# Kernel tuning notes

Measured on AMD Instinct MI355X. Metric: run time of the kernel, lower is better.

The kernel has to match this reference:

```python
import jax, jax.numpy as jnp
import numpy as np

GAMMA = 0.5

def _rbf_gram(a, b):
    # exp(-gamma * ||a - b||^2), computed via the expanded quadratic form.
    # a: [N, d], b: [M, d] -> [N, M]
    a2 = jnp.sum(a * a, axis=-1)                      # [N]
    b2 = jnp.sum(b * b, axis=-1)                      # [M]
    sq = a2[:, None] + b2[None, :] - 2.0 * (a @ b.T)  # [N, M]
    return jnp.exp(-GAMMA * jnp.maximum(sq, 0.0))


def setup_inputs() -> dict:
    key = jax.random.key(0)
    kx, kp = jax.random.split(key)
    x = jax.random.normal(kx, (32768, 16), dtype=jnp.float32)
    particles = jax.random.normal(kp, (8192, 16), dtype=jnp.float32)
    return {"x": x, "particles": particles}


def reference(x, particles):
    n_p = particles.shape[0]
    # p=None, norm=True -> px = ones(N_x) / N_x
    px = jnp.ones(x.shape[0], dtype=x.dtype) / x.shape[0]
    t1 = jnp.mean(_rbf_gram(particles, particles))           # mean over [N_p, N_p]
    t2 = 2.0 * jnp.sum(px @ _rbf_gram(x, particles)) / n_p   # weighted row-sum of [N_x, N_p]
    return t1 - t2
```

## Files before the change

### kernel.cpp

```cpp
#include <hip/hip_runtime.h>
#include <hip/hip_bf16.h>

#define THREADS 256
#define DIM 16

typedef __attribute__((ext_vector_type(8))) short bf16x8;
typedef __attribute__((ext_vector_type(16))) float f32x16;
typedef __attribute__((ext_vector_type(2))) float f32x2;

__device__ __forceinline__ float rawexp2(float a) { return __builtin_amdgcn_exp2f(a); }

__global__ __launch_bounds__(THREADS) void prep_kernel(
    const float* __restrict__ x, int nx,
    const float* __restrict__ p, int np,
    short* __restrict__ xbs, float* __restrict__ xn,
    short* __restrict__ pbs, short* __restrict__ pb,
    float* __restrict__ pn, float* __restrict__ pfp)
{
    const float L2E  = 1.44269504088896340736f;
    const float HL2E = 0.72134752044448170368f;
    int i = blockIdx.x * THREADS + threadIdx.x;
    const float* src; short* ds; short* dp; float* dn; float* df;
    if (i < nx) {
        src = x + (size_t)i * DIM; ds = xbs + (size_t)i * DIM;
        dp = nullptr; dn = xn + i; df = nullptr;
    } else if (i < nx + np) {
        int j = i - nx;
        src = p + (size_t)j * DIM; ds = pbs + (size_t)j * DIM;
        dp = pb + (size_t)j * DIM; dn = pn + j; df = pfp + j;
    } else {
        return;
    }

    float nrm = 0.f;
    bf16x8 plo, phi, slo, shi;
#pragma unroll
    for (int k = 0; k < DIM; ++k) {
        unsigned u = __float_as_uint(src[k]);
        unsigned short r = (unsigned short)((u + 0x7FFFu + ((u >> 16) & 1u)) >> 16);
        float fr = __uint_as_float((unsigned)r << 16);
        nrm = fmaf(fr, fr, nrm);
        unsigned us = __float_as_uint(L2E * fr);
        unsigned short rs = (unsigned short)((us + 0x7FFFu + ((us >> 16) & 1u)) >> 16);
        if (k < 8) { plo[k] = (short)r; slo[k] = (short)rs; }
        else       { phi[k - 8] = (short)r; shi[k - 8] = (short)rs; }
    }
    *(bf16x8*)ds = slo; *((bf16x8*)ds + 1) = shi;
    if (dp) { *(bf16x8*)dp = plo; *((bf16x8*)dp + 1) = phi; }
    float ns = -HL2E * nrm;
    *dn = ns;
    if (df) *df = rawexp2(ns);
}

__device__ __forceinline__ void consume_tile(const f32x16& d, float f, f32x2& acc)
{
    f32x2 e0 = { rawexp2(d[0]),  rawexp2(d[1])  };
    f32x2 e1 = { rawexp2(d[2]),  rawexp2(d[3])  };
    f32x2 e2 = { rawexp2(d[4]),  rawexp2(d[5])  };
    f32x2 e3 = { rawexp2(d[6]),  rawexp2(d[7])  };
    f32x2 e4 = { rawexp2(d[8]),  rawexp2(d[9])  };
    f32x2 e5 = { rawexp2(d[10]), rawexp2(d[11]) };
    f32x2 e6 = { rawexp2(d[12]), rawexp2(d[13]) };
    f32x2 e7 = { rawexp2(d[14]), rawexp2(d[15]) };

    f32x2 s0 = e0 + e1;
    f32x2 s1 = e2 + e3;
    f32x2 s2 = e4 + e5;
    f32x2 s3 = e6 + e7;
    f32x2 u0 = s0 + s1;
    f32x2 u1 = s2 + s3;
    f32x2 t  = u0 + u1;
    f32x2 pf2 = {f, f};
    acc = t * pf2 + acc;
}

__device__ __forceinline__ float gram_phase(
    const short* __restrict__ rowsb, const float* __restrict__ rown,
    const short* __restrict__ colsb, const float* __restrict__ colpf,
    int row0, int ct0, int ntiles, int l31, int half)
{
    bf16x8 afrag = *(const bf16x8*)(rowsb + (size_t)(row0 + l31) * DIM + half * 8);

    f32x16 cseed;
#pragma unroll
    for (int r = 0; r < 16; ++r) {
        int rrow = (r & 3) + 8 * (r >> 2) + 4 * half;
        cseed[r] = rown[row0 + rrow];
    }

    const short* bptr = colsb + ((size_t)ct0 * 32 + l31) * DIM + half * 8;
    const float* fptr = colpf + ct0 * 32 + l31;
    const size_t bstride = (size_t)32 * DIM;

    bf16x8 b0 = *(const bf16x8*)bptr;
    bf16x8 b1 = *(const bf16x8*)(bptr + bstride);
    float  f0 = fptr[0];
    float  f1 = fptr[32];

    f32x16 d0 = __builtin_amdgcn_mfma_f32_32x32x16_bf16(afrag, b0, cseed, 0, 0, 0);
    f32x16 d1 = __builtin_amdgcn_mfma_f32_32x32x16_bf16(afrag, b1, cseed, 0, 0, 0);

    f32x2 acc = {0.f, 0.f};

#pragma unroll 1
    for (int t = 0; t + 2 < ntiles; t += 2) {
        bf16x8 bn0 = *(const bf16x8*)(bptr + (size_t)(t + 2) * bstride);
        float  fn0 = fptr[(t + 2) * 32];
        bf16x8 bn1 = *(const bf16x8*)(bptr + (size_t)(t + 3) * bstride);
        float  fn1 = fptr[(t + 3) * 32];

        consume_tile(d0, f0, acc);
        d0 = __builtin_amdgcn_mfma_f32_32x32x16_bf16(afrag, bn0, cseed, 0, 0, 0);
        consume_tile(d1, f1, acc);
        d1 = __builtin_amdgcn_mfma_f32_32x32x16_bf16(afrag, bn1, cseed, 0, 0, 0);

        f0 = fn0; f1 = fn1;
    }
    consume_tile(d0, f0, acc);
    consume_tile(d1, f1, acc);
    return acc.x + acc.y;
}

__device__ __forceinline__ void tri_run(
    const short* __restrict__ rowsb, const float* __restrict__ rown,
    const short* __restrict__ colsb, const float* __restrict__ colpf,
    int rt, int ct0, int len, bool diagFirst, int l31, int half,
    f32x2& accD, f32x2& accU)
{
    if (len <= 0) return;
    const int row0 = rt * 32;
    bf16x8 afrag = *(const bf16x8*)(rowsb + (size_t)(row0 + l31) * DIM + half * 8);

    f32x16 cseed;
#pragma unroll
    for (int r = 0; r < 16; ++r) {
        int rrow = (r & 3) + 8 * (r >> 2) + 4 * half;
        cseed[r] = rown[row0 + rrow];
    }

    const short* bptr = colsb + ((size_t)ct0 * 32 + l31) * DIM + half * 8;
    const float* fptr = colpf + ct0 * 32 + l31;
    const size_t bstride = (size_t)32 * DIM;

    bf16x8 bC = *(const bf16x8*)bptr;
    float  fC = fptr[0];
    f32x16 d = __builtin_amdgcn_mfma_f32_32x32x16_bf16(afrag, bC, cseed, 0, 0, 0);

#pragma unroll 1
    for (int t = 0; t < len; ++t) {
        bf16x8 bN; float fN;
        if (t + 1 < len) {
            bN = *(const bf16x8*)(bptr + (size_t)(t + 1) * bstride);
            fN = fptr[(t + 1) * 32];
        }
        if (diagFirst && t == 0) {
            consume_tile(d, fC, accD);
        } else {
            consume_tile(d, fC, accU);
        }
        if (t + 1 < len) {
            d = __builtin_amdgcn_mfma_f32_32x32x16_bf16(afrag, bN, cseed, 0, 0, 0);
            fC = fN;
        }
    }
}

__global__ __launch_bounds__(THREADS) void gram_fused_kernel(
    const short* __restrict__ xbs, const float* __restrict__ xn,
    const short* __restrict__ pbs, const short* __restrict__ pb,
    const float* __restrict__ pn, const float* __restrict__ pfp,
    double sc1, double sc2,
    double* __restrict__ partials)
{
    const int lane = threadIdx.x & 63;
    const int wv   = threadIdx.x >> 6;
    const int l31  = lane & 31;
    const int half = lane >> 5;
    const int w    = blockIdx.x * (THREADS / 64) + wv;

    f32x2 accD = {0.f, 0.f}, accU = {0.f, 0.f};
    {
        const int j = w >> 5;
        const int k = w & 31;
        const int s   = (k == 0) ? 0 : 8 * k + 1;
        const int cnt = (k == 0) ? 9 : 8;
        const int m = 256 - j;

        {
            const int lo = s;
            const int hi = (s + cnt < m) ? (s + cnt) : m;
            const int lenA = hi - lo;
            if (lenA > 0)
                tri_run(pbs, pn, pb, pfp, j, j + lo, lenA, lo == 0,
                        l31, half, accD, accU);
        }
        {
            const int lo = (s > m) ? s : m;
            const int hi = s + cnt;
            const int lenB = hi - lo;
            if (lenB > 0) {
                const int i2 = lo - m;
                tri_run(pbs, pn, pb, pfp, 255 - j, (255 - j) + i2, lenB,
                        i2 == 0, l31, half, accD, accU);
            }
        }
    }
    float t1d = accD.x + accD.y;
    float t1u = accU.x + accU.y;

    const int rt2 = w & 1023;
    const int c20 = (w >> 10) * 64;
    float acc2 = gram_phase(xbs, xn, pb, pfp, rt2 * 32, c20, 64, l31, half);

    double v = ((double)t1d + 2.0 * (double)t1u) * sc1
             - (double)acc2 * sc2;
#pragma unroll
    for (int off = 32; off > 0; off >>= 1) v += __shfl_down(v, off);

    __shared__ double sred[THREADS / 64];
    if (lane == 0) sred[wv] = v;
    __syncthreads();
    if (threadIdx.x == 0) {
        double tot = 0.0;
#pragma unroll
        for (int q = 0; q < THREADS / 64; ++q) tot += sred[q];
        partials[blockIdx.x] = tot;
    }
}

__global__ __launch_bounds__(THREADS) void finalize_kernel(
    const double* __restrict__ partials, int n, float* __restrict__ out)
{
    double v = 0.0;
    for (int i = threadIdx.x; i < n; i += THREADS) v += partials[i];
#pragma unroll
    for (int off = 32; off > 0; off >>= 1) v += __shfl_down(v, off);

    __shared__ double sred[THREADS / 64];
    const int lane = threadIdx.x & 63;
    const int wid = threadIdx.x >> 6;
    if (lane == 0) sred[wid] = v;
    __syncthreads();
    if (threadIdx.x == 0) {
        double tot = 0.0;
#pragma unroll
        for (int q = 0; q < THREADS / 64; ++q) tot += sred[q];
        out[0] = (float)tot;
    }
}

extern "C" void kernel_launch(void* const* d_in, const int* in_sizes, int n_in,
                              void* d_out, int out_size, void* d_ws, size_t ws_size,
                              hipStream_t stream) {
    const float* x = (const float*)d_in[0];
    const float* particles = (const float*)d_in[1];
    float* out = (float*)d_out;

    const int NX = in_sizes[0] / DIM;
    const int NP = in_sizes[1] / DIM;

    const int NBLOCKS = 1024;

    char* ws = (char*)d_ws;
    double* partials = (double*)ws;
    float*  xn  = (float*)(ws + 16384);
    float*  pn  = (float*)(ws + 147456);
    float*  pfp = (float*)(ws + 180224);
    short*  xbs = (short*)(ws + 212992);
    short*  pbs = (short*)(ws + 1261568);
    short*  pb  = (short*)(ws + 1523712);

    const int nprep = (NX + NP + THREADS - 1) / THREADS;
    prep_kernel<<<nprep, THREADS, 0, stream>>>(x, NX, particles, NP,
                                               xbs, xn, pbs, pb, pn, pfp);

    gram_fused_kernel<<<NBLOCKS, THREADS, 0, stream>>>(
        xbs, xn, pbs, pb, pn, pfp,
        1.0 / ((double)NP * (double)NP),
        2.0 / ((double)NX * (double)NP),
        partials);

    finalize_kernel<<<1, THREADS, 0, stream>>>(partials, NBLOCKS, out);
}
```

Before: 47.34 us.

## Fuse finalize into gram kernel via last-block atomic, double-buffer triangle tiles

```diff
diff --git a/kernel.cpp b/kernel.cpp
--- a/kernel.cpp
+++ b/kernel.cpp
@@ -3,6 +3,7 @@
 
 #define THREADS 256
 #define DIM 16
+#define NBLOCKS 1024
 
 typedef __attribute__((ext_vector_type(8))) short bf16x8;
 typedef __attribute__((ext_vector_type(16))) float f32x16;
@@ -15,11 +16,13 @@
     const float* __restrict__ p, int np,
     short* __restrict__ xbs, float* __restrict__ xn,
     short* __restrict__ pbs, short* __restrict__ pb,
-    float* __restrict__ pn, float* __restrict__ pfp)
+    float* __restrict__ pn, float* __restrict__ pfp,
+    unsigned* __restrict__ counter)
 {
     const float L2E  = 1.44269504088896340736f;
     const float HL2E = 0.72134752044448170368f;
     int i = blockIdx.x * THREADS + threadIdx.x;
+    if (i == 0) *counter = 0u;
     const float* src; short* ds; short* dp; float* dn; float* df;
     if (i < nx) {
         src = x + (size_t)i * DIM; ds = xbs + (size_t)i * DIM;
@@ -102,7 +105,7 @@
 
     f32x2 acc = {0.f, 0.f};
 
-#pragma unroll 1
+#pragma unroll 2
     for (int t = 0; t + 2 < ntiles; t += 2) {
         bf16x8 bn0 = *(const bf16x8*)(bptr + (size_t)(t + 2) * bstride);
         float  fn0 = fptr[(t + 2) * 32];
@@ -142,26 +145,49 @@
     const float* fptr = colpf + ct0 * 32 + l31;
     const size_t bstride = (size_t)32 * DIM;
 
-    bf16x8 bC = *(const bf16x8*)bptr;
-    float  fC = fptr[0];
-    f32x16 d = __builtin_amdgcn_mfma_f32_32x32x16_bf16(afrag, bC, cseed, 0, 0, 0);
-
+    if (len == 1) {
+        bf16x8 b = *(const bf16x8*)bptr;
+        float  f = fptr[0];
+        f32x16 d = __builtin_amdgcn_mfma_f32_32x32x16_bf16(afrag, b, cseed, 0, 0, 0);
+        if (diagFirst) consume_tile(d, f, accD); else consume_tile(d, f, accU);
+        return;
+    }
+
+    bf16x8 b0 = *(const bf16x8*)bptr;
+    float  f0 = fptr[0];
+    bf16x8 b1 = *(const bf16x8*)(bptr + bstride);
+    float  f1 = fptr[32];
+    f32x16 d0 = __builtin_amdgcn_mfma_f32_32x32x16_bf16(afrag, b0, cseed, 0, 0, 0);
+    f32x16 d1 = __builtin_amdgcn_mfma_f32_32x32x16_bf16(afrag, b1, cseed, 0, 0, 0);
+
+    int t = 0;
 #pragma unroll 1
-    for (int t = 0; t < len; ++t) {
-        bf16x8 bN; float fN;
-        if (t + 1 < len) {
-            bN = *(const bf16x8*)(bptr + (size_t)(t + 1) * bstride);
-            fN = fptr[(t + 1) * 32];
-        }
-        if (diagFirst && t == 0) {
-            consume_tile(d, fC, accD);
-        } else {
-            consume_tile(d, fC, accU);
-        }
-        if (t + 1 < len) {
-            d = __builtin_amdgcn_mfma_f32_32x32x16_bf16(afrag, bN, cseed, 0, 0, 0);
-            fC = fN;
-        }
+    for (; t + 3 < len; t += 2) {
+        bf16x8 bn0 = *(const bf16x8*)(bptr + (size_t)(t + 2) * bstride);
+        float  fn0 = fptr[(t + 2) * 32];
+        bf16x8 bn1 = *(const bf16x8*)(bptr + (size_t)(t + 3) * bstride);
+        float  fn1 = fptr[(t + 3) * 32];
+
+        if (diagFirst && t == 0) consume_tile(d0, f0, accD);
+        else                     consume_tile(d0, f0, accU);
+        d0 = __builtin_amdgcn_mfma_f32_32x32x16_bf16(afrag, bn0, cseed, 0, 0, 0);
+        consume_tile(d1, f1, accU);
+        d1 = __builtin_amdgcn_mfma_f32_32x32x16_bf16(afrag, bn1, cseed, 0, 0, 0);
+
+        f0 = fn0; f1 = fn1;
+    }
+    if (len - t == 3) {
+        bf16x8 bn0 = *(const bf16x8*)(bptr + (size_t)(t + 2) * bstride);
+        float  fn0 = fptr[(t + 2) * 32];
+        if (diagFirst && t == 0) consume_tile(d0, f0, accD);
+        else                     consume_tile(d0, f0, accU);
+        d0 = __builtin_amdgcn_mfma_f32_32x32x16_bf16(afrag, bn0, cseed, 0, 0, 0);
+        consume_tile(d1, f1, accU);
+        consume_tile(d0, fn0, accU);
+    } else {
+        if (diagFirst && t == 0) consume_tile(d0, f0, accD);
+        else                     consume_tile(d0, f0, accU);
+        consume_tile(d1, f1, accU);
     }
 }
 
@@ -170,7 +196,8 @@
     const short* __restrict__ pbs, const short* __restrict__ pb,
     const float* __restrict__ pn, const float* __restrict__ pfp,
     double sc1, double sc2,
-    double* __restrict__ partials)
+    double* __restrict__ partials, unsigned* __restrict__ counter,
+    float* __restrict__ out)
 {
     const int lane = threadIdx.x & 63;
     const int wv   = threadIdx.x >> 6;
@@ -218,6 +245,7 @@
     for (int off = 32; off > 0; off >>= 1) v += __shfl_down(v, off);
 
     __shared__ double sred[THREADS / 64];
+    __shared__ bool isLast;
     if (lane == 0) sred[wv] = v;
     __syncthreads();
     if (threadIdx.x == 0) {
@@ -225,27 +253,26 @@
 #pragma unroll
         for (int q = 0; q < THREADS / 64; ++q) tot += sred[q];
         partials[blockIdx.x] = tot;
-    }
-}
-
-__global__ __launch_bounds__(THREADS) void finalize_kernel(
-    const double* __restrict__ partials, int n, float* __restrict__ out)
-{
-    double v = 0.0;
-    for (int i = threadIdx.x; i < n; i += THREADS) v += partials[i];
-#pragma unroll
-    for (int off = 32; off > 0; off >>= 1) v += __shfl_down(v, off);
-
-    __shared__ double sred[THREADS / 64];
-    const int lane = threadIdx.x & 63;
-    const int wid = threadIdx.x >> 6;
-    if (lane == 0) sred[wid] = v;
+        __threadfence();
+        unsigned prev = atomicAdd(counter, 1u);
+        isLast = (prev == (unsigned)(gridDim.x - 1));
+    }
     __syncthreads();
-    if (threadIdx.x == 0) {
-        double tot = 0.0;
-#pragma unroll
-        for (int q = 0; q < THREADS / 64; ++q) tot += sred[q];
-        out[0] = (float)tot;
+
+    if (isLast) {
+        __threadfence();
+        double r = 0.0;
+        for (int i = threadIdx.x; i < NBLOCKS; i += THREADS) r += partials[i];
+#pragma unroll
+        for (int off = 32; off > 0; off >>= 1) r += __shfl_down(r, off);
+        if (lane == 0) sred[wv] = r;
+        __syncthreads();
+        if (threadIdx.x == 0) {
+            double tot = 0.0;
+#pragma unroll
+            for (int q = 0; q < THREADS / 64; ++q) tot += sred[q];
+            out[0] = (float)tot;
+        }
     }
 }
 
@@ -259,10 +286,9 @@
     const int NX = in_sizes[0] / DIM;
     const int NP = in_sizes[1] / DIM;
 
-    const int NBLOCKS = 1024;
-
     char* ws = (char*)d_ws;
-    double* partials = (double*)ws;
+    double*   partials = (double*)ws;
+    unsigned* counter  = (unsigned*)(ws + 8192);
     float*  xn  = (float*)(ws + 16384);
     float*  pn  = (float*)(ws + 147456);
     float*  pfp = (float*)(ws + 180224);
@@ -272,13 +298,12 @@
 
     const int nprep = (NX + NP + THREADS - 1) / THREADS;
     prep_kernel<<<nprep, THREADS, 0, stream>>>(x, NX, particles, NP,
-                                               xbs, xn, pbs, pb, pn, pfp);
+                                               xbs, xn, pbs, pb, pn, pfp,
+                                               counter);
 
     gram_fused_kernel<<<NBLOCKS, THREADS, 0, stream>>>(
         xbs, xn, pbs, pb, pn, pfp,
         1.0 / ((double)NP * (double)NP),
         2.0 / ((double)NX * (double)NP),
-        partials);
-
-    finalize_kernel<<<1, THREADS, 0, stream>>>(partials, NBLOCKS, out);
-}
+        partials, counter, out);
+}
```

New measurement: 60.64 us. +28.1%, slower.
